# Performance work log

Measured on AMD Instinct MI355X. Metric: run time of the kernel, lower is better.

Reference implementation:

```python
import jax, jax.numpy as jnp
import numpy as np

DIM = 32      # state dim (enc_shape[0])
LDIM = 256    # latent dim (enc_shape[-1])
N_AUX = LDIM // 2
AUX_H = 128   # aux hidden
ENC_H = 256   # encoder hidden
T = 64        # n_shifts
N = 1024      # batch
DT = 0.01


def setup_inputs() -> dict:
    key = jax.random.key(0)
    ks = jax.random.split(key, 13)
    def w(k, shape, fan):
        return jax.random.normal(k, shape, jnp.float32) / np.sqrt(fan).astype(np.float32)
    return {
        "xs": jax.random.normal(ks[0], (N, T, DIM), jnp.float32),
        # encoder MLP: dim -> 256 -> 256 -> ldim (last layer has no bias)
        "enc_W1": w(ks[1], (DIM, ENC_H), DIM), "enc_b1": w(ks[2], (ENC_H,), ENC_H),
        "enc_W2": w(ks[3], (ENC_H, ENC_H), ENC_H), "enc_b2": w(ks[4], (ENC_H,), ENC_H),
        "enc_W3": w(ks[5], (ENC_H, LDIM), ENC_H),
        # n_aux independent aux MLPs: dim -> 128 -> 128 -> 2 (last no bias), stacked
        "aux_W1": w(ks[6], (N_AUX, DIM, AUX_H), DIM), "aux_b1": w(ks[7], (N_AUX, AUX_H), AUX_H),
        "aux_W2": w(ks[8], (N_AUX, AUX_H, AUX_H), AUX_H), "aux_b2": w(ks[9], (N_AUX, AUX_H), AUX_H),
        "aux_W3": w(ks[10], (N_AUX, AUX_H, 2), AUX_H),
        # C: Linear(ldim, dim, bias=False); stored as [ldim, dim] so x_next = y @ C_W
        "C_W": w(ks[11], (LDIM, DIM), LDIM),
    }


def reference(xs, enc_W1, enc_b1, enc_W2, enc_b2, enc_W3,
              aux_W1, aux_b1, aux_W2, aux_b2, aux_W3, C_W):
    x0 = xs[:, 0, :]                                    # [N, dim]
    # all n_aux tiny MLPs batched via einsum (instead of python loop)
    h = jax.nn.relu(jnp.einsum('nd,kdh->nkh', x0, aux_W1) + aux_b1)
    h = jax.nn.relu(jnp.einsum('nkh,khg->nkg', h, aux_W2) + aux_b2)
    aux = jnp.einsum('nkh,kho->nko', h, aux_W3)          # [N, n_aux, 2] -> (mu, omega)
    scale = jnp.exp(aux[..., 0] * DT)
    cos = jnp.cos(aux[..., 1] * DT) * scale              # [N, n_aux]
    sin = jnp.sin(aux[..., 1] * DT) * scale

    # encoder over all n_shifts timesteps
    e = jax.nn.relu(xs @ enc_W1 + enc_b1)
    e = jax.nn.relu(e @ enc_W2 + enc_b2)
    e = e @ enc_W3                                       # [N, T, ldim]
    y = jnp.concatenate([xs, e], axis=-1)                # [N, T, dim+ldim]

    # Koopman recurrence. The original builds a block-diagonal [ldim, ldim]
    # matrix of 2x2 rotation-scaling blocks (block k acts on latent pair
    # (2k, 2k+1)) and applies it as a row-vector bmm: out = y_row @ K with
    # K_block = [[cos, sin], [-sin, cos]]. We apply the blocks directly.
    y0 = e[:, 0, :].reshape(N, N_AUX, 2)
    def step(carry, _):
        y1, y2 = carry[..., 0], carry[..., 1]
        yn = jnp.stack([y1 * cos - y2 * sin, y1 * sin + y2 * cos], axis=-1)
        return yn, yn
    _, ys = jax.lax.scan(step, y0, None, length=T - 1)   # [T-1, N, n_aux, 2]
    ys = jnp.moveaxis(ys, 0, 1).reshape(N, T - 1, LDIM)  # [N, T-1, ldim]

    y_lat = jnp.concatenate([e[:, :1, :], ys], axis=1)          # [N, T, ldim]
    x_pred = jnp.concatenate([xs[:, :1, :], ys @ C_W], axis=1)  # [N, T, dim]
    y_pred = jnp.concatenate([x_pred, y_lat], axis=-1)          # [N, T, dim+ldim]
    return y, y_pred
```

## Files before the change

### kernel.cpp

```cpp
#include <hip/hip_runtime.h>
#include <math.h>

#define N_SEQ 1024
#define T_SEQ 64
#define DIMX  32
#define LDIM  256
#define NAUX  128
#define AUXH  128
#define ENCH  256
#define OUTC  288
#define DT    0.01f

typedef short bf16x8 __attribute__((ext_vector_type(8)));
typedef float f32x4  __attribute__((ext_vector_type(4)));
typedef unsigned short ush;

__device__ __forceinline__ ush f2bf(float f) {
    unsigned u = __builtin_bit_cast(unsigned, f);
    unsigned r = u + 0x7fffu + ((u >> 16) & 1u);
    return (ush)(r >> 16);
}
__device__ __forceinline__ float bf2f(ush h) {
    unsigned u = ((unsigned)h) << 16;
    return __builtin_bit_cast(float, u);
}
__device__ __forceinline__ f32x4 mfma16(bf16x8 a, bf16x8 b, f32x4 c) {
    return __builtin_amdgcn_mfma_f32_16x16x32_bf16(a, b, c, 0, 0, 0);
}

#define CV_ENC   139264
#define PREP_CONV_BLOCKS 576
#define PREP_TR_BLOCKS   2560
#define PREP_ENC0_BLOCKS 256
__global__ __launch_bounds__(256) void prep_kernel(
    const float* __restrict__ eW1, const float* __restrict__ eb1,
    const float* __restrict__ eW2, const float* __restrict__ eb2,
    const float* __restrict__ eW3, const float* __restrict__ C_W,
    const float* __restrict__ aW1, const float* __restrict__ aW2,
    const float* __restrict__ xs,
    ush* __restrict__ encw, float* __restrict__ cwt,
    ush* __restrict__ a1h, ush* __restrict__ a1l,
    ush* __restrict__ a2h, ush* __restrict__ a2l,
    float* __restrict__ y)
{
    __shared__ float psm[1152];
    const int b   = blockIdx.x;
    const int tid = threadIdx.x;

    if (b < PREP_CONV_BLOCKS) {
        const int idx = b * 256 + tid;
        if (idx < 8192) {
            int c = idx >> 5, k = idx & 31;
            encw[idx] = f2bf(eW1[k * ENCH + c]);
        } else if (idx < 8192 + 65536) {
            int t = idx - 8192; int c = t >> 8, k = t & 255;
            encw[idx] = f2bf(eW2[k * ENCH + c]);
        } else if (idx < CV_ENC) {
            int t = idx - (8192 + 65536); int c = t >> 8, k = t & 255;
            encw[idx] = f2bf(eW3[k * LDIM + c]);
        } else if (idx < CV_ENC + 8192) {
            int t = idx - CV_ENC; int d = t >> 8, l = t & 255;
            cwt[t] = C_W[l * DIMX + d];
        }
        return;
    }

    if (b < PREP_CONV_BLOCKS + PREP_TR_BLOCKS) {
        float (*tile)[33] = (float(*)[33])psm;
        const int bb0 = b - PREP_CONV_BLOCKS;
        const float* src; ush *dh, *dl; int R, j0, r0;
        if (bb0 < 512) {
            int k = bb0 >> 2; j0 = (bb0 & 3) * 32; r0 = 0; R = 32;
            src = aW1 + (size_t)k * 4096;
            dh = a1h + (size_t)k * 4096; dl = a1l + (size_t)k * 4096;
        } else {
            int bb = bb0 - 512;
            int k = bb >> 4; j0 = ((bb >> 2) & 3) * 32; r0 = (bb & 3) * 32; R = 128;
            src = aW2 + (size_t)k * 16384;
            dh = a2h + (size_t)k * 16384; dl = a2l + (size_t)k * 16384;
        }
        for (int i = tid; i < 1024; i += 256) {
            int rr = i >> 5, jj = i & 31;
            tile[rr][jj] = src[(r0 + rr) * 128 + j0 + jj];
        }
        __syncthreads();
        for (int i = tid; i < 1024; i += 256) {
            int jj = i >> 5, rr = i & 31;
            float w = tile[rr][jj];
            ush hi = f2bf(w);
            int off = (j0 + jj) * R + r0 + rr;
            dh[off] = hi;
            dl[off] = f2bf(w - bf2f(hi));
        }
        return;
    }

    {
        float* Xs  = psm;
        float* Hsf = psm + 128;
        const int c  = tid;
        const int n0 = (b - PREP_CONV_BLOCKS - PREP_TR_BLOCKS) * 4;

        if (tid < 32) {
            int r = tid >> 3, q = tid & 7;
            *(float4*)&Xs[r * 32 + q * 4] =
                *(const float4*)&xs[(size_t)(n0 + r) * (T_SEQ * DIMX) + q * 4];
        }
        __syncthreads();

        float acc[4];
        {
            float w[32];
            #pragma unroll
            for (int d = 0; d < 32; ++d) w[d] = eW1[d * ENCH + c];
            const float bb = eb1[c];
            #pragma unroll
            for (int r = 0; r < 4; ++r) {
                float a = bb;
                #pragma unroll
                for (int d4 = 0; d4 < 8; ++d4) {
                    float4 xv = *(const float4*)&Xs[r * 32 + d4 * 4];
                    a += xv.x * w[d4*4] + xv.y * w[d4*4+1] + xv.z * w[d4*4+2] + xv.w * w[d4*4+3];
                }
                acc[r] = a;
            }
            #pragma unroll
            for (int r = 0; r < 4; ++r) Hsf[r * 256 + c] = fmaxf(acc[r], 0.f);
        }
        __syncthreads();
        {
            const float bb = eb2[c];
            #pragma unroll
            for (int r = 0; r < 4; ++r) acc[r] = bb;
            for (int hc = 0; hc < 8; ++hc) {
                float w[32];
                #pragma unroll
                for (int i = 0; i < 32; ++i) w[i] = eW2[(hc * 32 + i) * ENCH + c];
                #pragma unroll
                for (int r = 0; r < 4; ++r) {
                    float a = acc[r];
                    #pragma unroll
                    for (int h4 = 0; h4 < 8; ++h4) {
                        float4 hv = *(const float4*)&Hsf[r * 256 + hc * 32 + h4 * 4];
                        a += hv.x * w[h4*4] + hv.y * w[h4*4+1] + hv.z * w[h4*4+2] + hv.w * w[h4*4+3];
                    }
                    acc[r] = a;
                }
            }
            __syncthreads();
            #pragma unroll
            for (int r = 0; r < 4; ++r) Hsf[r * 256 + c] = fmaxf(acc[r], 0.f);
        }
        __syncthreads();
        {
            #pragma unroll
            for (int r = 0; r < 4; ++r) acc[r] = 0.f;
            for (int hc = 0; hc < 8; ++hc) {
                float w[32];
                #pragma unroll
                for (int i = 0; i < 32; ++i) w[i] = eW3[(hc * 32 + i) * LDIM + c];
                #pragma unroll
                for (int r = 0; r < 4; ++r) {
                    float a = acc[r];
                    #pragma unroll
                    for (int h4 = 0; h4 < 8; ++h4) {
                        float4 hv = *(const float4*)&Hsf[r * 256 + hc * 32 + h4 * 4];
                        a += hv.x * w[h4*4] + hv.y * w[h4*4+1] + hv.z * w[h4*4+2] + hv.w * w[h4*4+3];
                    }
                    acc[r] = a;
                }
            }
        }
        #pragma unroll
        for (int r = 0; r < 4; ++r)
            y[((size_t)(n0 + r) * T_SEQ) * OUTC + DIMX + c] = acc[r];
    }
}

__global__ __launch_bounds__(256) void auxm_kernel(
    const float* __restrict__ xs,
    const ush* __restrict__ W1h, const ush* __restrict__ W1l,
    const float* __restrict__ b1,
    const ush* __restrict__ W2h, const ush* __restrict__ W2l,
    const float* __restrict__ b2,
    const float* __restrict__ W3,
    float* __restrict__ a_ws, float* __restrict__ th_ws)
{
    const int k   = blockIdx.x >> 5;
    const int n0  = (blockIdx.x & 31) << 5;
    const int tid = threadIdx.x;
    const int wv  = tid >> 6;
    const int ln  = tid & 63;
    const int lr  = ln & 15;
    const int g   = ln >> 4;
    const int cb  = wv * 32;

    __shared__ ush   x0h[32][40];
    __shared__ ush   x0l[32][40];
    __shared__ ush   h1h[32][136];
    __shared__ ush   h1l[32][136];
    __shared__ float w3s[256];
    __shared__ float p3[256];

    for (int i = tid; i < 256; i += 256) {
        int r = i >> 3, qd = i & 7;
        float4 v = *(const float4*)&xs[(size_t)(n0 + r) * (T_SEQ * DIMX) + qd * 4];
        short4 hs, ls;
        float vv[4] = {v.x, v.y, v.z, v.w};
        short* hp = (short*)&hs; short* lp = (short*)&ls;
        #pragma unroll
        for (int u = 0; u < 4; ++u) {
            ush hi = f2bf(vv[u]);
            hp[u] = (short)hi;
            lp[u] = (short)f2bf(vv[u] - bf2f(hi));
        }
        *(short4*)&x0h[r][qd * 4] = hs;
        *(short4*)&x0l[r][qd * 4] = ls;
    }
    w3s[tid] = W3[(size_t)k * (AUXH * 2) + tid];
    __syncthreads();

    {
        const ush* W1hk = W1h + (size_t)k * 4096;
        const ush* W1lk = W1l + (size_t)k * 4096;
        bf16x8 bh[2], bl[2];
        #pragma unroll
        for (int ct = 0; ct < 2; ++ct) {
            int off = (cb + ct * 16 + lr) * 32 + g * 8;
            bh[ct] = *(const bf16x8*)&W1hk[off];
            bl[ct] = *(const bf16x8*)&W1lk[off];
        }
        f32x4 acc[2][2];
        #pragma unroll
        for (int rt = 0; rt < 2; ++rt) {
            bf16x8 ah = *(const bf16x8*)&x0h[rt * 16 + lr][g * 8];
            bf16x8 al = *(const bf16x8*)&x0l[rt * 16 + lr][g * 8];
            #pragma unroll
            for (int ct = 0; ct < 2; ++ct) {
                f32x4 z = {0.f, 0.f, 0.f, 0.f};
                z = mfma16(ah, bl[ct], z);
                z = mfma16(al, bh[ct], z);
                acc[rt][ct] = mfma16(ah, bh[ct], z);
            }
        }
        #pragma unroll
        for (int ct = 0; ct < 2; ++ct) {
            const int col = cb + ct * 16 + lr;
            const float bb = b1[k * 128 + col];
            #pragma unroll
            for (int rt = 0; rt < 2; ++rt)
                #pragma unroll
                for (int i = 0; i < 4; ++i) {
                    float h = fmaxf(acc[rt][ct][i] + bb, 0.f);
                    ush hi = f2bf(h);
                    int row = rt * 16 + g * 4 + i;
                    h1h[row][col] = hi;
                    h1l[row][col] = f2bf(h - bf2f(hi));
                }
        }
    }
    __syncthreads();

    {
        const ush* W2hk = W2h + (size_t)k * 16384;
        const ush* W2lk = W2l + (size_t)k * 16384;
        f32x4 acc[2][2];
        #pragma unroll
        for (int rt = 0; rt < 2; ++rt)
            #pragma unroll
            for (int ct = 0; ct < 2; ++ct) acc[rt][ct] = (f32x4){0.f,0.f,0.f,0.f};

        #pragma unroll
        for (int kk = 0; kk < 4; ++kk) {
            bf16x8 bh[2], bl[2], ah[2], al[2];
            #pragma unroll
            for (int ct = 0; ct < 2; ++ct) {
                int off = (cb + ct * 16 + lr) * 128 + kk * 32 + g * 8;
                bh[ct] = *(const bf16x8*)&W2hk[off];
                bl[ct] = *(const bf16x8*)&W2lk[off];
            }
            #pragma unroll
            for (int rt = 0; rt < 2; ++rt) {
                ah[rt] = *(const bf16x8*)&h1h[rt * 16 + lr][kk * 32 + g * 8];
                al[rt] = *(const bf16x8*)&h1l[rt * 16 + lr][kk * 32 + g * 8];
            }
            #pragma unroll
            for (int rt = 0; rt < 2; ++rt)
                #pragma unroll
                for (int ct = 0; ct < 2; ++ct) {
                    f32x4 z = acc[rt][ct];
                    z = mfma16(ah[rt], bl[ct], z);
                    z = mfma16(al[rt], bh[ct], z);
                    acc[rt][ct] = mfma16(ah[rt], bh[ct], z);
                }
        }
        __syncthreads();
        #pragma unroll
        for (int ct = 0; ct < 2; ++ct) {
            const int col = cb + ct * 16 + lr;
            const float bb = b2[k * 128 + col];
            #pragma unroll
            for (int rt = 0; rt < 2; ++rt)
                #pragma unroll
                for (int i = 0; i < 4; ++i) {
                    float h = fmaxf(acc[rt][ct][i] + bb, 0.f);
                    ush hi = f2bf(h);
                    int row = rt * 16 + g * 4 + i;
                    h1h[row][col] = hi;
                    h1l[row][col] = f2bf(h - bf2f(hi));
                }
        }
    }
    __syncthreads();

    {
        const int n = tid >> 3, o = (tid >> 2) & 1, q = tid & 3;
        float s = 0.f;
        #pragma unroll
        for (int h8 = q * 32; h8 < q * 32 + 32; h8 += 8) {
            bf16x8 vh = *(const bf16x8*)&h1h[n][h8];
            bf16x8 vl = *(const bf16x8*)&h1l[n][h8];
            #pragma unroll
            for (int u = 0; u < 8; ++u) {
                float hv = bf2f((ush)vh[u]) + bf2f((ush)vl[u]);
                s += hv * w3s[(h8 + u) * 2 + o];
            }
        }
        p3[tid] = s;
    }
    __syncthreads();
    if (tid < 64) {
        const int n = tid >> 1, o = tid & 1;
        const int base = n * 8 + o * 4;
        float v = (p3[base] + p3[base + 1] + p3[base + 2] + p3[base + 3]) * DT;
        float* dst = o ? th_ws : a_ws;
        dst[(size_t)(n0 + n) * NAUX + k] = v;
    }
}

__global__ __launch_bounds__(256) void encm_kernel(
    const float* __restrict__ xs,
    const ush* __restrict__ W1T, const float* __restrict__ b1,
    const ush* __restrict__ W2T, const float* __restrict__ b2,
    const ush* __restrict__ W3T,
    float* __restrict__ y)
{
    __shared__ float Xf[64 * 36];
    __shared__ ush   Hs[64 * 264];

    const int tid = threadIdx.x;
    const int wv  = tid >> 6;
    const int ln  = tid & 63;
    const int lr  = ln & 15;
    const int g   = ln >> 4;
    const int cb  = wv * 64;
    const size_t row0 = (size_t)blockIdx.x * 64;

    {
        const float4* src = (const float4*)(xs + row0 * DIMX);
        for (int i = tid; i < 512; i += 256) {
            int r = i >> 3, q = i & 7;
            *(float4*)&Xf[r * 36 + q * 4] = src[i];
        }
    }
    __syncthreads();

    {
        f32x4 acc[4][4];
        bf16x8 bfr[4], afr[4];
        #pragma unroll
        for (int ct = 0; ct < 4; ++ct)
            bfr[ct] = *(const bf16x8*)&W1T[(cb + ct * 16 + lr) * 32 + g * 8];
        #pragma unroll
        for (int rt = 0; rt < 4; ++rt) {
            const float* xp = &Xf[(rt * 16 + lr) * 36 + g * 8];
            float4 u = *(const float4*)xp;
            float4 v = *(const float4*)(xp + 4);
            bf16x8 t;
            t[0]=(short)f2bf(u.x); t[1]=(short)f2bf(u.y); t[2]=(short)f2bf(u.z); t[3]=(short)f2bf(u.w);
            t[4]=(short)f2bf(v.x); t[5]=(short)f2bf(v.y); t[6]=(short)f2bf(v.z); t[7]=(short)f2bf(v.w);
            afr[rt] = t;
        }
        #pragma unroll
        for (int rt = 0; rt < 4; ++rt)
            #pragma unroll
            for (int ct = 0; ct < 4; ++ct) {
                f32x4 z = {0.f, 0.f, 0.f, 0.f};
                acc[rt][ct] = mfma16(afr[rt], bfr[ct], z);
            }
        #pragma unroll
        for (int ct = 0; ct < 4; ++ct) {
            const float bb = b1[cb + ct * 16 + lr];
            #pragma unroll
            for (int rt = 0; rt < 4; ++rt)
                #pragma unroll
                for (int i = 0; i < 4; ++i) {
                    float h = fmaxf(acc[rt][ct][i] + bb, 0.f);
                    Hs[(rt * 16 + g * 4 + i) * 264 + cb + ct * 16 + lr] = f2bf(h);
                }
        }
    }
    __syncthreads();

    int wrow[4], hoff[4];
    #pragma unroll
    for (int ct = 0; ct < 4; ++ct) wrow[ct] = (cb + ct * 16 + lr) * 256 + g * 8;
    #pragma unroll
    for (int rt = 0; rt < 4; ++rt) hoff[rt] = (rt * 16 + lr) * 264 + g * 8;

    {
        f32x4 acc[4][4];
        #pragma unroll
        for (int rt = 0; rt < 4; ++rt)
            #pragma unroll
            for (int ct = 0; ct < 4; ++ct) acc[rt][ct] = (f32x4){0.f,0.f,0.f,0.f};
        #pragma unroll 2
        for (int kk = 0; kk < 8; ++kk) {
            bf16x8 bfr[4], afr[4];
            #pragma unroll
            for (int ct = 0; ct < 4; ++ct)
                bfr[ct] = *(const bf16x8*)&W2T[wrow[ct] + kk * 32];
            #pragma unroll
            for (int rt = 0; rt < 4; ++rt)
                afr[rt] = *(const bf16x8*)&Hs[hoff[rt] + kk * 32];
            #pragma unroll
            for (int rt = 0; rt < 4; ++rt)
                #pragma unroll
                for (int ct = 0; ct < 4; ++ct)
                    acc[rt][ct] = mfma16(afr[rt], bfr[ct], acc[rt][ct]);
        }
        __syncthreads();
        #pragma unroll
        for (int ct = 0; ct < 4; ++ct) {
            const float bb = b2[cb + ct * 16 + lr];
            #pragma unroll
            for (int rt = 0; rt < 4; ++rt)
                #pragma unroll
                for (int i = 0; i < 4; ++i) {
                    float h = fmaxf(acc[rt][ct][i] + bb, 0.f);
                    Hs[(rt * 16 + g * 4 + i) * 264 + cb + ct * 16 + lr] = f2bf(h);
                }
        }
    }
    __syncthreads();

    {
        f32x4 acc[4][4];
        #pragma unroll
        for (int rt = 0; rt < 4; ++rt)
            #pragma unroll
            for (int ct = 0; ct < 4; ++ct) acc[rt][ct] = (f32x4){0.f,0.f,0.f,0.f};
        #pragma unroll 2
        for (int kk = 0; kk < 8; ++kk) {
            bf16x8 bfr[4], afr[4];
            #pragma unroll
            for (int ct = 0; ct < 4; ++ct)
                bfr[ct] = *(const bf16x8*)&W3T[wrow[ct] + kk * 32];
            #pragma unroll
            for (int rt = 0; rt < 4; ++rt)
                afr[rt] = *(const bf16x8*)&Hs[hoff[rt] + kk * 32];
            #pragma unroll
            for (int rt = 0; rt < 4; ++rt)
                #pragma unroll
                for (int ct = 0; ct < 4; ++ct)
                    acc[rt][ct] = mfma16(afr[rt], bfr[ct], acc[rt][ct]);
        }
        __syncthreads();

        float* HsF = (float*)Hs;
        const int r  = tid >> 3;
        const int ce = tid & 7;

        #pragma unroll
        for (int p = 0; p < 2; ++p) {
            #pragma unroll
            for (int rt = 2 * p; rt < 2 * p + 2; ++rt)
                #pragma unroll
                for (int ct = 0; ct < 4; ++ct)
                    #pragma unroll
                    for (int i = 0; i < 4; ++i)
                        HsF[((rt - 2 * p) * 16 + g * 4 + i) * 264 + cb + ct * 16 + lr]
                            = acc[rt][ct][i];
            __syncthreads();
            const int rloc = p * 32 + r;
            float* dstrow = &y[(row0 + rloc) * OUTC];
            #pragma unroll
            for (int j = 0; j < 9; ++j) {
                int f4 = j * 8 + ce;
                float4 v;
                if (f4 < 8) v = *(const float4*)&Xf[rloc * 36 + f4 * 4];
                else        v = *(const float4*)&HsF[r * 264 + (f4 - 8) * 4];
                if (!(rloc == 0 && f4 >= 8))
                    *(float4*)&dstrow[f4 * 4] = v;
            }
            __syncthreads();
        }
    }
}

__global__ __launch_bounds__(256) void scan3_kernel(
    const float* __restrict__ xs,
    const float* __restrict__ a_ws, const float* __restrict__ th_ws,
    const float* __restrict__ cwt,
    const float* __restrict__ y,
    float* __restrict__ yp)
{
    __shared__ float ys_lds[16][256];

    const int n = blockIdx.x >> 2;
    const int q = blockIdx.x & 3;
    const int e = threadIdx.x;
    const int k = e >> 1;

    const float* yrow0 = y + (size_t)n * T_SEQ * OUTC + DIMX;
    float2 y0 = *(const float2*)&yrow0[e & ~1];
    const float a  = a_ws [n * NAUX + k];
    const float th = th_ws[n * NAUX + k];

    const float m = expf(a);
    float ss, cc; sincosf(th, &ss, &cc);
    const float zr = m * cc, zi = m * ss;

    float pr = zr, pi = zi;
    #pragma unroll
    for (int s2 = 0; s2 < 4; ++s2) {
        float nr = pr * pr - pi * pi;
        pi = 2.f * pr * pi; pr = nr;
    }
    float wr = 1.f, wi = 0.f;
    for (int j = 0; j < q; ++j) {
        float nr = wr * pr - wi * pi;
        wi = wr * pi + wi * pr; wr = nr;
    }

    const bool imag = e & 1;
    float* ypn = yp + (size_t)n * T_SEQ * OUTC;

    #pragma unroll 4
    for (int tl = 0; tl < 16; ++tl) {
        const int t = q * 16 + tl;
        float val = imag ? (y0.x * wi + y0.y * wr)
                         : (y0.x * wr - y0.y * wi);
        ypn[(size_t)t * OUTC + DIMX + e] = val;
        ys_lds[tl][(e + ((tl >> 1) & 7) * 4) & 255] = val;
        float nwr = wr * zr - wi * zi;
        wi = wr * zi + wi * zr;
        wr = nwr;
    }
    __syncthreads();

    const int d   = e >> 3;
    const int tg  = e & 7;
    const int tl0 = tg * 2, tl1 = tl0 + 1;
    const float* cwd = cwt + d * 256;
    const int rot = tg * 4;

    float s0 = 0.f, s1 = 0.f;
    #pragma unroll 8
    for (int l = 0; l < 256; l += 4) {
        const int c0 = (l + rot) & 255;
        float4 wv = *(const float4*)&cwd[l];
        float4 ya = *(const float4*)&ys_lds[tl0][c0];
        float4 yb = *(const float4*)&ys_lds[tl1][c0];
        s0 += ya.x * wv.x + ya.y * wv.y + ya.z * wv.z + ya.w * wv.w;
        s1 += yb.x * wv.x + yb.y * wv.y + yb.z * wv.z + yb.w * wv.w;
    }
    const int t0 = q * 16 + tl0;
    const int t1 = q * 16 + tl1;
    float o0 = (t0 == 0) ? xs[(size_t)n * T_SEQ * DIMX + d] : s0;
    ypn[(size_t)t0 * OUTC + d] = o0;
    ypn[(size_t)t1 * OUTC + d] = s1;
}

extern "C" void kernel_launch(void* const* d_in, const int* in_sizes, int n_in,
                              void* d_out, int out_size, void* d_ws, size_t ws_size,
                              hipStream_t stream)
{
    const float* xs   = (const float*)d_in[0];
    const float* eW1  = (const float*)d_in[1];
    const float* eb1  = (const float*)d_in[2];
    const float* eW2  = (const float*)d_in[3];
    const float* eb2  = (const float*)d_in[4];
    const float* eW3  = (const float*)d_in[5];
    const float* aW1  = (const float*)d_in[6];
    const float* ab1  = (const float*)d_in[7];
    const float* aW2  = (const float*)d_in[8];
    const float* ab2  = (const float*)d_in[9];
    const float* aW3  = (const float*)d_in[10];
    const float* C_W  = (const float*)d_in[11];

    float* y  = (float*)d_out;
    float* yp = y + (size_t)N_SEQ * T_SEQ * OUTC;

    float* a_ws  = (float*)d_ws;
    float* th_ws = a_ws + (size_t)N_SEQ * NAUX;
    ush* encw = (ush*)(th_ws + (size_t)N_SEQ * NAUX);
    ush* W1T = encw;
    ush* W2T = encw + 8192;
    ush* W3T = encw + 8192 + 65536;
    ush* a1h = encw + CV_ENC;
    ush* a1l = a1h + 524288;
    ush* a2h = a1l + 524288;
    ush* a2l = a2h + 2097152;
    float* cwt = (float*)(a2l + 2097152);

    prep_kernel<<<PREP_CONV_BLOCKS + PREP_TR_BLOCKS + PREP_ENC0_BLOCKS, 256, 0, stream>>>(
        eW1, eb1, eW2, eb2, eW3, C_W, aW1, aW2, xs,
        encw, cwt, a1h, a1l, a2h, a2l, y);
    auxm_kernel<<<128 * 32, 256, 0, stream>>>(
        xs, a1h, a1l, ab1, a2h, a2l, ab2, aW3, a_ws, th_ws);
    encm_kernel<<<N_SEQ * T_SEQ / 64, 256, 0, stream>>>(
        xs, W1T, eb1, W2T, eb2, W3T, y);
    scan3_kernel<<<N_SEQ * 4, 256, 0, stream>>>(xs, a_ws, th_ws, cwt, y, yp);
}
```

Baseline: 172.3 us.

## Hold aux MLP weights in registers and loop over batch tiles per block

The aux MLP kernel now launches 512 blocks instead of 4096. Each block loads one aux network's W1/W2 hi/lo fragments into registers once, then loops over four 64-row batch tiles, where before each block handled 32 rows. This cuts repeated global weight loads and per-block setup, and doubles the MFMA work per tile. The costs are much higher register pressure (w2 fragments held across the loop), less parallelism for latency hiding, and larger shared memory tiles.

```diff
diff --git a/kernel.cpp b/kernel.cpp
--- a/kernel.cpp
+++ b/kernel.cpp
@@ -186,8 +186,8 @@
     const float* __restrict__ W3,
     float* __restrict__ a_ws, float* __restrict__ th_ws)
 {
-    const int k   = blockIdx.x >> 5;
-    const int n0  = (blockIdx.x & 31) << 5;
+    const int k   = blockIdx.x >> 2;
+    const int qn  = blockIdx.x & 3;
     const int tid = threadIdx.x;
     const int wv  = tid >> 6;
     const int ln  = tid & 63;
@@ -195,146 +195,156 @@
     const int g   = ln >> 4;
     const int cb  = wv * 32;
 
-    __shared__ ush   x0h[32][40];
-    __shared__ ush   x0l[32][40];
-    __shared__ ush   h1h[32][136];
-    __shared__ ush   h1l[32][136];
+    __shared__ ush   x0h[64][40];
+    __shared__ ush   x0l[64][40];
+    __shared__ ush   h1h[64][136];
+    __shared__ ush   h1l[64][136];
     __shared__ float w3s[256];
     __shared__ float p3[256];
 
-    for (int i = tid; i < 256; i += 256) {
-        int r = i >> 3, qd = i & 7;
-        float4 v = *(const float4*)&xs[(size_t)(n0 + r) * (T_SEQ * DIMX) + qd * 4];
-        short4 hs, ls;
-        float vv[4] = {v.x, v.y, v.z, v.w};
-        short* hp = (short*)&hs; short* lp = (short*)&ls;
-        #pragma unroll
-        for (int u = 0; u < 4; ++u) {
-            ush hi = f2bf(vv[u]);
-            hp[u] = (short)hi;
-            lp[u] = (short)f2bf(vv[u] - bf2f(hi));
-        }
-        *(short4*)&x0h[r][qd * 4] = hs;
-        *(short4*)&x0l[r][qd * 4] = ls;
-    }
-    w3s[tid] = W3[(size_t)k * (AUXH * 2) + tid];
-    __syncthreads();
-
+    bf16x8 w1bh[2], w1bl[2], w2bh[4][2], w2bl[4][2];
     {
         const ush* W1hk = W1h + (size_t)k * 4096;
         const ush* W1lk = W1l + (size_t)k * 4096;
-        bf16x8 bh[2], bl[2];
         #pragma unroll
         for (int ct = 0; ct < 2; ++ct) {
             int off = (cb + ct * 16 + lr) * 32 + g * 8;
-            bh[ct] = *(const bf16x8*)&W1hk[off];
-            bl[ct] = *(const bf16x8*)&W1lk[off];
-        }
-        f32x4 acc[2][2];
-        #pragma unroll
-        for (int rt = 0; rt < 2; ++rt) {
-            bf16x8 ah = *(const bf16x8*)&x0h[rt * 16 + lr][g * 8];
-            bf16x8 al = *(const bf16x8*)&x0l[rt * 16 + lr][g * 8];
-            #pragma unroll
-            for (int ct = 0; ct < 2; ++ct) {
-                f32x4 z = {0.f, 0.f, 0.f, 0.f};
-                z = mfma16(ah, bl[ct], z);
-                z = mfma16(al, bh[ct], z);
-                acc[rt][ct] = mfma16(ah, bh[ct], z);
-            }
-        }
-        #pragma unroll
-        for (int ct = 0; ct < 2; ++ct) {
-            const int col = cb + ct * 16 + lr;
-            const float bb = b1[k * 128 + col];
-            #pragma unroll
-            for (int rt = 0; rt < 2; ++rt)
-                #pragma unroll
-                for (int i = 0; i < 4; ++i) {
-                    float h = fmaxf(acc[rt][ct][i] + bb, 0.f);
-                    ush hi = f2bf(h);
-                    int row = rt * 16 + g * 4 + i;
-                    h1h[row][col] = hi;
-                    h1l[row][col] = f2bf(h - bf2f(hi));
-                }
-        }
-    }
-    __syncthreads();
-
-    {
+            w1bh[ct] = *(const bf16x8*)&W1hk[off];
+            w1bl[ct] = *(const bf16x8*)&W1lk[off];
+        }
         const ush* W2hk = W2h + (size_t)k * 16384;
         const ush* W2lk = W2l + (size_t)k * 16384;
-        f32x4 acc[2][2];
-        #pragma unroll
-        for (int rt = 0; rt < 2; ++rt)
-            #pragma unroll
-            for (int ct = 0; ct < 2; ++ct) acc[rt][ct] = (f32x4){0.f,0.f,0.f,0.f};
-
-        #pragma unroll
-        for (int kk = 0; kk < 4; ++kk) {
-            bf16x8 bh[2], bl[2], ah[2], al[2];
+        #pragma unroll
+        for (int kk = 0; kk < 4; ++kk)
             #pragma unroll
             for (int ct = 0; ct < 2; ++ct) {
                 int off = (cb + ct * 16 + lr) * 128 + kk * 32 + g * 8;
-                bh[ct] = *(const bf16x8*)&W2hk[off];
-                bl[ct] = *(const bf16x8*)&W2lk[off];
-            }
-            #pragma unroll
-            for (int rt = 0; rt < 2; ++rt) {
-                ah[rt] = *(const bf16x8*)&h1h[rt * 16 + lr][kk * 32 + g * 8];
-                al[rt] = *(const bf16x8*)&h1l[rt * 16 + lr][kk * 32 + g * 8];
-            }
-            #pragma unroll
-            for (int rt = 0; rt < 2; ++rt)
+                w2bh[kk][ct] = *(const bf16x8*)&W2hk[off];
+                w2bl[kk][ct] = *(const bf16x8*)&W2lk[off];
+            }
+    }
+    w3s[tid] = W3[(size_t)k * (AUXH * 2) + tid];
+
+    const float bb1[2] = { b1[k * 128 + cb + lr], b1[k * 128 + cb + 16 + lr] };
+    const float bb2[2] = { b2[k * 128 + cb + lr], b2[k * 128 + cb + 16 + lr] };
+
+    for (int t8 = 0; t8 < 4; ++t8) {
+        const int n0 = qn * 256 + t8 * 64;
+        __syncthreads();
+
+        for (int i = tid; i < 512; i += 256) {
+            int r = i >> 3, qd = i & 7;
+            float4 v = *(const float4*)&xs[(size_t)(n0 + r) * (T_SEQ * DIMX) + qd * 4];
+            short4 hs, ls;
+            float vv[4] = {v.x, v.y, v.z, v.w};
+            short* hp = (short*)&hs; short* lp = (short*)&ls;
+            #pragma unroll
+            for (int u = 0; u < 4; ++u) {
+                ush hi = f2bf(vv[u]);
+                hp[u] = (short)hi;
+                lp[u] = (short)f2bf(vv[u] - bf2f(hi));
+            }
+            *(short4*)&x0h[r][qd * 4] = hs;
+            *(short4*)&x0l[r][qd * 4] = ls;
+        }
+        __syncthreads();
+
+        {
+            f32x4 acc[4][2];
+            #pragma unroll
+            for (int rt = 0; rt < 4; ++rt) {
+                bf16x8 ah = *(const bf16x8*)&x0h[rt * 16 + lr][g * 8];
+                bf16x8 al = *(const bf16x8*)&x0l[rt * 16 + lr][g * 8];
                 #pragma unroll
                 for (int ct = 0; ct < 2; ++ct) {
-                    f32x4 z = acc[rt][ct];
-                    z = mfma16(ah[rt], bl[ct], z);
-                    z = mfma16(al[rt], bh[ct], z);
-                    acc[rt][ct] = mfma16(ah[rt], bh[ct], z);
-                }
-        }
-        __syncthreads();
-        #pragma unroll
-        for (int ct = 0; ct < 2; ++ct) {
-            const int col = cb + ct * 16 + lr;
-            const float bb = b2[k * 128 + col];
-            #pragma unroll
-            for (int rt = 0; rt < 2; ++rt)
-                #pragma unroll
-                for (int i = 0; i < 4; ++i) {
-                    float h = fmaxf(acc[rt][ct][i] + bb, 0.f);
-                    ush hi = f2bf(h);
-                    int row = rt * 16 + g * 4 + i;
-                    h1h[row][col] = hi;
-                    h1l[row][col] = f2bf(h - bf2f(hi));
-                }
-        }
-    }
-    __syncthreads();
-
-    {
-        const int n = tid >> 3, o = (tid >> 2) & 1, q = tid & 3;
-        float s = 0.f;
-        #pragma unroll
-        for (int h8 = q * 32; h8 < q * 32 + 32; h8 += 8) {
-            bf16x8 vh = *(const bf16x8*)&h1h[n][h8];
-            bf16x8 vl = *(const bf16x8*)&h1l[n][h8];
-            #pragma unroll
-            for (int u = 0; u < 8; ++u) {
-                float hv = bf2f((ush)vh[u]) + bf2f((ush)vl[u]);
-                s += hv * w3s[(h8 + u) * 2 + o];
-            }
-        }
-        p3[tid] = s;
-    }
-    __syncthreads();
-    if (tid < 64) {
-        const int n = tid >> 1, o = tid & 1;
-        const int base = n * 8 + o * 4;
-        float v = (p3[base] + p3[base + 1] + p3[base + 2] + p3[base + 3]) * DT;
-        float* dst = o ? th_ws : a_ws;
-        dst[(size_t)(n0 + n) * NAUX + k] = v;
+                    f32x4 z = {0.f, 0.f, 0.f, 0.f};
+                    z = mfma16(ah, w1bl[ct], z);
+                    z = mfma16(al, w1bh[ct], z);
+                    acc[rt][ct] = mfma16(ah, w1bh[ct], z);
+                }
+            }
+            #pragma unroll
+            for (int ct = 0; ct < 2; ++ct) {
+                const int col = cb + ct * 16 + lr;
+                #pragma unroll
+                for (int rt = 0; rt < 4; ++rt)
+                    #pragma unroll
+                    for (int i = 0; i < 4; ++i) {
+                        float h = fmaxf(acc[rt][ct][i] + bb1[ct], 0.f);
+                        ush hi = f2bf(h);
+                        int row = rt * 16 + g * 4 + i;
+                        h1h[row][col] = hi;
+                        h1l[row][col] = f2bf(h - bf2f(hi));
+                    }
+            }
+        }
+        __syncthreads();
+
+        {
+            f32x4 acc[4][2];
+            #pragma unroll
+            for (int rt = 0; rt < 4; ++rt)
+                #pragma unroll
+                for (int ct = 0; ct < 2; ++ct) acc[rt][ct] = (f32x4){0.f,0.f,0.f,0.f};
+
+            #pragma unroll
+            for (int kk = 0; kk < 4; ++kk) {
+                bf16x8 ah[4], al[4];
+                #pragma unroll
+                for (int rt = 0; rt < 4; ++rt) {
+                    ah[rt] = *(const bf16x8*)&h1h[rt * 16 + lr][kk * 32 + g * 8];
+                    al[rt] = *(const bf16x8*)&h1l[rt * 16 + lr][kk * 32 + g * 8];
+                }
+                #pragma unroll
+                for (int rt = 0; rt < 4; ++rt)
+                    #pragma unroll
+                    for (int ct = 0; ct < 2; ++ct) {
+                        f32x4 z = acc[rt][ct];
+                        z = mfma16(ah[rt], w2bl[kk][ct], z);
+                        z = mfma16(al[rt], w2bh[kk][ct], z);
+                        acc[rt][ct] = mfma16(ah[rt], w2bh[kk][ct], z);
+                    }
+            }
+            __syncthreads();
+            #pragma unroll
+            for (int ct = 0; ct < 2; ++ct) {
+                const int col = cb + ct * 16 + lr;
+                #pragma unroll
+                for (int rt = 0; rt < 4; ++rt)
+                    #pragma unroll
+                    for (int i = 0; i < 4; ++i) {
+                        float h = fmaxf(acc[rt][ct][i] + bb2[ct], 0.f);
+                        ush hi = f2bf(h);
+                        int row = rt * 16 + g * 4 + i;
+                        h1h[row][col] = hi;
+                        h1l[row][col] = f2bf(h - bf2f(hi));
+                    }
+            }
+        }
+        __syncthreads();
+
+        {
+            const int hh = tid >> 7, r = tid & 127, n = r >> 1, o = r & 1;
+            float s = 0.f;
+            #pragma unroll
+            for (int h8 = hh * 64; h8 < hh * 64 + 64; h8 += 8) {
+                bf16x8 vh = *(const bf16x8*)&h1h[n][h8];
+                bf16x8 vl = *(const bf16x8*)&h1l[n][h8];
+                #pragma unroll
+                for (int u = 0; u < 8; ++u) {
+                    float hv = bf2f((ush)vh[u]) + bf2f((ush)vl[u]);
+                    s += hv * w3s[(h8 + u) * 2 + o];
+                }
+            }
+            p3[tid] = s;
+        }
+        __syncthreads();
+        if (tid < 128) {
+            const int n = tid >> 1, o = tid & 1;
+            float v = (p3[tid] + p3[tid + 128]) * DT;
+            float* dst = o ? th_ws : a_ws;
+            dst[(size_t)(n0 + n) * NAUX + k] = v;
+        }
     }
 }
 
@@ -607,7 +617,7 @@
     prep_kernel<<<PREP_CONV_BLOCKS + PREP_TR_BLOCKS + PREP_ENC0_BLOCKS, 256, 0, stream>>>(
         eW1, eb1, eW2, eb2, eW3, C_W, aW1, aW2, xs,
         encw, cwt, a1h, a1l, a2h, a2l, y);
-    auxm_kernel<<<128 * 32, 256, 0, stream>>>(
+    auxm_kernel<<<512, 256, 0, stream>>>(
         xs, a1h, a1l, ab1, a2h, a2l, ab2, aW3, a_ws, th_ws);
     encm_kernel<<<N_SEQ * T_SEQ / 64, 256, 0, stream>>>(
         xs, W1T, eb1, W2T, eb2, W3T, y);
```

Result: faster. 162.7 us (-5.5%).
